# Kernel optimization log

Measured on AMD Instinct MI355X. Metric: run time of the kernel, lower is better.

The kernel has to match this reference:

```python
import jax, jax.numpy as jnp
import numpy as np
import math

T, B, E, H = 1024, 4, 512, 8
HD = E // H

def setup_inputs() -> dict:
    key = jax.random.key(0)
    ks = jax.random.split(key, 6)
    return {
        "query": jax.random.normal(ks[0], (T, B, E), dtype=jnp.float32),
        "dist": jax.random.normal(ks[1], (B, T, T, H), dtype=jnp.float32) * 0.1,
        "in_proj_weight": jax.random.normal(ks[2], (3 * E, E), dtype=jnp.float32) * 0.02,
        "in_proj_bias": jax.random.normal(ks[3], (3 * E,), dtype=jnp.float32) * 0.02,
        "out_proj_weight": jax.random.normal(ks[4], (E, E), dtype=jnp.float32) * 0.02,
        "out_proj_bias": jax.random.normal(ks[5], (E,), dtype=jnp.float32) * 0.02,
    }

def reference(query, dist, in_proj_weight, in_proj_bias, out_proj_weight, out_proj_bias):
    t, b, e = query.shape
    # packed in-projection (self-attention: q=k=v=query)
    qkv = query @ in_proj_weight.T + in_proj_bias          # [T,B,3E]
    q, k, v = jnp.split(qkv, 3, axis=-1)                   # each [T,B,E]
    def heads(x):
        return x.reshape(t, b * H, HD).transpose(1, 0, 2)  # [B*H,T,HD]
    q, k, v = heads(q), heads(k), heads(v)
    q = q / math.sqrt(HD)
    attn = jnp.einsum('bte,bse->bts', q, k)                # [B*H,T,T]
    # distance/structure bias: [B,T,T,H] -> [B,H,T,T] -> [B*H,T,T]
    bias = jnp.transpose(dist, (0, 3, 1, 2)).reshape(b * H, t, t)
    attn = jax.nn.softmax(attn + bias, axis=-1)
    out = jnp.einsum('bts,bse->bte', attn, v)              # [B*H,T,HD]
    out = out.transpose(1, 0, 2).reshape(t, b, e)          # [T,B,E]
    out = out @ out_proj_weight.T + out_proj_bias
    return out
```

## Files before the change

### kernel.cpp

```cpp
#include <hip/hip_runtime.h>
#include <math.h>

typedef __bf16 bf16;
typedef bf16 bf16x8 __attribute__((ext_vector_type(8)));
typedef bf16 bf16x4 __attribute__((ext_vector_type(4)));
typedef float f32x4 __attribute__((ext_vector_type(4)));

#define T_DIM 1024
#define B_DIM 4
#define E_DIM 512
#define H_DIM 8
#define HD_DIM 64
#define BH_DIM 32
#define SPLIT 4
#define S_PER (T_DIM / SPLIT)

__device__ __forceinline__ f32x4 mfma16(bf16x8 a, bf16x8 b, f32x4 c) {
    return __builtin_amdgcn_mfma_f32_16x16x32_bf16(a, b, c, 0, 0, 0);
}

__device__ __forceinline__ bf16x4 cvt4(f32x4 v) {
    bf16x4 o;
    o[0] = (bf16)v[0]; o[1] = (bf16)v[1]; o[2] = (bf16)v[2]; o[3] = (bf16)v[3];
    return o;
}

#define CVT_Q_V   524288
#define CVT_W1_V  196608
__global__ __launch_bounds__(256)
void cvt_all(const float* __restrict__ q, const float* __restrict__ w1,
             const float* __restrict__ w2, bf16* __restrict__ qo,
             bf16* __restrict__ w1o, bf16* __restrict__ w2o) {
    long v = (long)blockIdx.x * 256 + threadIdx.x;
    const float* src; bf16* dst;
    if (v < CVT_Q_V)                { src = q;  dst = qo; }
    else if (v < CVT_Q_V + CVT_W1_V){ v -= CVT_Q_V;  src = w1; dst = w1o; }
    else                            { v -= CVT_Q_V + CVT_W1_V; src = w2; dst = w2o; }
    f32x4 f = *(const f32x4*)(src + v * 4);
    *(bf16x4*)(dst + v * 4) = cvt4(f);
}

__global__ __launch_bounds__(256)
void bias_transpose(const float* __restrict__ dist, bf16* __restrict__ bias_t) {
    __shared__ __align__(16) bf16 tile[8 * 1032];
    const int bt = blockIdx.x;
    const int b = bt >> 10, t = bt & 1023;
    const int tid = threadIdx.x;
    const float* src = dist + ((long)bt << 13) + tid * 32;
    const int s0 = tid * 4;
    float v[32];
#pragma unroll
    for (int j = 0; j < 8; j++) {
        f32x4 f = *(const f32x4*)(src + j * 4);
        v[j * 4 + 0] = f[0]; v[j * 4 + 1] = f[1];
        v[j * 4 + 2] = f[2]; v[j * 4 + 3] = f[3];
    }
#pragma unroll
    for (int h = 0; h < 8; h++)
#pragma unroll
        for (int si = 0; si < 4; si++)
            tile[h * 1032 + s0 + si] = (bf16)v[si * 8 + h];
    __syncthreads();
#pragma unroll
    for (int rep = 0; rep < 4; rep++) {
        int slot = rep * 256 + tid;
        int h = slot >> 7;
        int sc = (slot & 127) * 8;
        bf16x8 o = *(const bf16x8*)&tile[h * 1032 + sc];
        *(bf16x8*)&bias_t[((long)(b * 8 + h) * T_DIM + t) * T_DIM + sc] = o;
    }
}

template<int TM, int TN, int MODE>
__global__ __launch_bounds__(256)
void gemm_t(const bf16* __restrict__ A, const bf16* __restrict__ Bt,
            const float* __restrict__ bias, int K, int N,
            float* __restrict__ out, bf16* __restrict__ qb,
            bf16* __restrict__ kb, bf16* __restrict__ vb) {
    constexpr int FM = TM / 32, FN = TN / 32;
    constexpr int PA = TM / 64, PB = TN / 64;
    __shared__ __align__(16) bf16 As[TM * 72];
    __shared__ __align__(16) bf16 Bs[TN * 72];
    const int tid  = threadIdx.x;
    const int lane = tid & 63;
    const int wave = tid >> 6;
    const int quad = lane >> 4;
    const int l15  = lane & 15;
    const int wm = wave & 1, wn = wave >> 1;
    const int m0 = blockIdx.x * TM, n0 = blockIdx.y * TN;

    f32x4 acc[FM][FN] = {};

    const int sr = tid >> 2;
    const int sc = (tid & 3) * 16;

    bf16x8 ra[PA][2], rb[PB][2];
#pragma unroll
    for (int p = 0; p < PA; p++) {
        const bf16* src = &A[(long)(m0 + p * 64 + sr) * K + sc];
        ra[p][0] = *(const bf16x8*)(src);
        ra[p][1] = *(const bf16x8*)(src + 8);
    }
#pragma unroll
    for (int p = 0; p < PB; p++) {
        const bf16* src = &Bt[(long)(n0 + p * 64 + sr) * K + sc];
        rb[p][0] = *(const bf16x8*)(src);
        rb[p][1] = *(const bf16x8*)(src + 8);
    }

    for (int k0 = 0; k0 < K; k0 += 64) {
        __syncthreads();
#pragma unroll
        for (int p = 0; p < PA; p++) {
            *(bf16x8*)&As[(p * 64 + sr) * 72 + sc]     = ra[p][0];
            *(bf16x8*)&As[(p * 64 + sr) * 72 + sc + 8] = ra[p][1];
        }
#pragma unroll
        for (int p = 0; p < PB; p++) {
            *(bf16x8*)&Bs[(p * 64 + sr) * 72 + sc]     = rb[p][0];
            *(bf16x8*)&Bs[(p * 64 + sr) * 72 + sc + 8] = rb[p][1];
        }
        __syncthreads();

        if (k0 + 64 < K) {
            const int kn = k0 + 64;
#pragma unroll
            for (int p = 0; p < PA; p++) {
                const bf16* src = &A[(long)(m0 + p * 64 + sr) * K + kn + sc];
                ra[p][0] = *(const bf16x8*)(src);
                ra[p][1] = *(const bf16x8*)(src + 8);
            }
#pragma unroll
            for (int p = 0; p < PB; p++) {
                const bf16* src = &Bt[(long)(n0 + p * 64 + sr) * K + kn + sc];
                rb[p][0] = *(const bf16x8*)(src);
                rb[p][1] = *(const bf16x8*)(src + 8);
            }
        }

#pragma unroll
        for (int kk = 0; kk < 64; kk += 32) {
            bf16x8 af[FM], bfr[FN];
#pragma unroll
            for (int mb = 0; mb < FM; mb++)
                af[mb] = *(const bf16x8*)&As[(wm * (TM / 2) + mb * 16 + l15) * 72 + kk + quad * 8];
#pragma unroll
            for (int nb = 0; nb < FN; nb++)
                bfr[nb] = *(const bf16x8*)&Bs[(wn * (TN / 2) + nb * 16 + l15) * 72 + kk + quad * 8];
#pragma unroll
            for (int mb = 0; mb < FM; mb++)
#pragma unroll
                for (int nb = 0; nb < FN; nb++)
                    acc[mb][nb] = mfma16(af[mb], bfr[nb], acc[mb][nb]);
        }
    }

#pragma unroll
    for (int mb = 0; mb < FM; mb++) {
#pragma unroll
        for (int nb = 0; nb < FN; nb++) {
            int n = n0 + wn * (TN / 2) + nb * 16 + l15;
            float bv = bias[n];
#pragma unroll
            for (int r = 0; r < 4; r++) {
                int m = m0 + wm * (TM / 2) + mb * 16 + quad * 4 + r;
                float v = acc[mb][nb][r] + bv;
                if (MODE == 0) {
                    out[(long)m * N + n] = v;
                } else {
                    int t = m >> 2, b = m & 3;
                    int sec = n >> 9, j = n & 511;
                    int h = j >> 6, hd = j & 63;
                    int bh = b * 8 + h;
                    if (sec == 0)
                        qb[((long)bh * T_DIM + t) * HD_DIM + hd] = (bf16)(v * 0.125f);
                    else if (sec == 1)
                        kb[((long)bh * T_DIM + t) * HD_DIM + hd] = (bf16)v;
                    else
                        vb[((long)bh * HD_DIM + hd) * T_DIM + t] = (bf16)v;
                }
            }
        }
    }
}

__global__ __launch_bounds__(256)
void attn_kernel(const bf16* __restrict__ qb, const bf16* __restrict__ kb,
                 const bf16* __restrict__ vb, const bf16* __restrict__ bias_t,
                 float* __restrict__ po, float* __restrict__ pl) {
    __shared__ __align__(16) bf16 Ks[64 * 72];
    __shared__ __align__(16) bf16 Vts[64 * 72];
    __shared__ __align__(16) bf16 Ps[4 * 16 * 72];
    const int tid  = threadIdx.x;
    const int lane = tid & 63;
    const int wave = tid >> 6;
    const int quad = lane >> 4;
    const int l15  = lane & 15;
    const int bid  = blockIdx.x;
    const int bh   = (bid >> 4) & 31;
    const int qt   = bid & 15;
    const int split = bid >> 9;
    const int s0   = split * S_PER;
    const int b    = bh >> 3;
    const int qrow = qt * 64 + wave * 16 + l15;

    bf16x8 qa0 = *(const bf16x8*)&qb[((long)bh * T_DIM + qrow) * HD_DIM + quad * 8];
    bf16x8 qa1 = *(const bf16x8*)&qb[((long)bh * T_DIM + qrow) * HD_DIM + 32 + quad * 8];

    f32x4 oacc[4] = {};
    float lsum[4] = {0.f, 0.f, 0.f, 0.f};

    const int r0 = tid >> 3;
    const int c0 = (tid & 7) * 8;

    const bf16* dp = bias_t + ((long)bh * T_DIM + qt * 64 + wave * 16 + quad * 4) * T_DIM;

    bf16x8 pk0, pk1, pv0, pv1;
    float pbias[16];
    pk0 = *(const bf16x8*)&kb[((long)bh * T_DIM + s0 + r0) * HD_DIM + c0];
    pk1 = *(const bf16x8*)&kb[((long)bh * T_DIM + s0 + r0 + 32) * HD_DIM + c0];
    pv0 = *(const bf16x8*)&vb[((long)bh * HD_DIM + r0) * T_DIM + s0 + c0];
    pv1 = *(const bf16x8*)&vb[((long)bh * HD_DIM + r0 + 32) * T_DIM + s0 + c0];
#pragma unroll
    for (int r = 0; r < 4; r++)
#pragma unroll
        for (int nb = 0; nb < 4; nb++)
            pbias[r * 4 + nb] = (float)dp[(long)r * T_DIM + s0 + nb * 16 + l15];

    for (int st = s0; st < s0 + S_PER; st += 64) {
        __syncthreads();
        *(bf16x8*)&Ks[r0 * 72 + c0]         = pk0;
        *(bf16x8*)&Ks[(r0 + 32) * 72 + c0]  = pk1;
        *(bf16x8*)&Vts[r0 * 72 + c0]        = pv0;
        *(bf16x8*)&Vts[(r0 + 32) * 72 + c0] = pv1;
        __syncthreads();

        if (st + 64 < s0 + S_PER) {
            const int sn = st + 64;
            pk0 = *(const bf16x8*)&kb[((long)bh * T_DIM + sn + r0) * HD_DIM + c0];
            pk1 = *(const bf16x8*)&kb[((long)bh * T_DIM + sn + r0 + 32) * HD_DIM + c0];
            pv0 = *(const bf16x8*)&vb[((long)bh * HD_DIM + r0) * T_DIM + sn + c0];
            pv1 = *(const bf16x8*)&vb[((long)bh * HD_DIM + r0 + 32) * T_DIM + sn + c0];
        }

        f32x4 sacc[4] = {};
        __builtin_amdgcn_s_setprio(1);
#pragma unroll
        for (int kk = 0; kk < 64; kk += 32) {
            bf16x8 a = (kk == 0) ? qa0 : qa1;
#pragma unroll
            for (int nb = 0; nb < 4; nb++) {
                bf16x8 bfr = *(const bf16x8*)&Ks[(nb * 16 + l15) * 72 + kk + quad * 8];
                sacc[nb] = mfma16(a, bfr, sacc[nb]);
            }
        }
        __builtin_amdgcn_s_setprio(0);

        bf16* pw = &Ps[wave * 16 * 72];
#pragma unroll
        for (int r = 0; r < 4; r++) {
            float rs = 0.f;
#pragma unroll
            for (int nb = 0; nb < 4; nb++) {
                float p = __expf(sacc[nb][r] + pbias[r * 4 + nb]);
                rs += p;
                pw[(quad * 4 + r) * 72 + nb * 16 + l15] = (bf16)p;
            }
            lsum[r] += rs;
        }

        if (st + 64 < s0 + S_PER) {
            const int sn = st + 64;
#pragma unroll
            for (int r = 0; r < 4; r++)
#pragma unroll
                for (int nb = 0; nb < 4; nb++)
                    pbias[r * 4 + nb] = (float)dp[(long)r * T_DIM + sn + nb * 16 + l15];
        }

        __builtin_amdgcn_s_setprio(1);
#pragma unroll
        for (int kk = 0; kk < 64; kk += 32) {
            bf16x8 ap = *(const bf16x8*)&pw[l15 * 72 + kk + quad * 8];
#pragma unroll
            for (int nb = 0; nb < 4; nb++) {
                bf16x8 bv2 = *(const bf16x8*)&Vts[(nb * 16 + l15) * 72 + kk + quad * 8];
                oacc[nb] = mfma16(ap, bv2, oacc[nb]);
            }
        }
        __builtin_amdgcn_s_setprio(0);
    }

#pragma unroll
    for (int r = 0; r < 4; r++) {
#pragma unroll
        for (int msk = 1; msk < 16; msk <<= 1)
            lsum[r] += __shfl_xor(lsum[r], msk);
    }

    float* pob = po + (long)split * (BH_DIM * T_DIM * HD_DIM);
#pragma unroll
    for (int nb = 0; nb < 4; nb++) {
#pragma unroll
        for (int r = 0; r < 4; r++) {
            int t  = qt * 64 + wave * 16 + quad * 4 + r;
            int hd = nb * 16 + l15;
            pob[((long)bh * T_DIM + t) * HD_DIM + hd] = oacc[nb][r];
        }
    }
    if (l15 == 0) {
#pragma unroll
        for (int r = 0; r < 4; r++) {
            int t = qt * 64 + wave * 16 + quad * 4 + r;
            pl[(long)split * (BH_DIM * T_DIM) + bh * T_DIM + t] = lsum[r];
        }
    }
}

__global__ __launch_bounds__(256)
void combine(const float* __restrict__ po, const float* __restrict__ pl,
             bf16* __restrict__ ctxb) {
    const int gid = blockIdx.x * 256 + threadIdx.x;
    const int hd4 = gid & 15;
    const int t   = (gid >> 4) & 1023;
    const int bh  = gid >> 14;
    const long base = ((long)bh * T_DIM + t) * HD_DIM + hd4 * 4;
    f32x4 o = {};
    float l = 0.f;
#pragma unroll
    for (int s = 0; s < SPLIT; s++) {
        o += *(const f32x4*)&po[(long)s * (BH_DIM * T_DIM * HD_DIM) + base];
        l += pl[(long)s * (BH_DIM * T_DIM) + bh * T_DIM + t];
    }
    float inv = 1.f / l;
    f32x4 r = o * inv;
    const int b = bh >> 3, hh = bh & 7;
    *(bf16x4*)&ctxb[((long)t * B_DIM + b) * E_DIM + hh * HD_DIM + hd4 * 4] = cvt4(r);
}

extern "C" void kernel_launch(void* const* d_in, const int* in_sizes, int n_in,
                              void* d_out, int out_size, void* d_ws, size_t ws_size,
                              hipStream_t stream) {
    const float* query = (const float*)d_in[0];
    const float* dist  = (const float*)d_in[1];
    const float* win   = (const float*)d_in[2];
    const float* bin   = (const float*)d_in[3];
    const float* wout  = (const float*)d_in[4];
    const float* bout  = (const float*)d_in[5];
    float* out = (float*)d_out;

    bf16* bias_t = (bf16*)d_ws;
    bf16* qb   = bias_t + ((long)BH_DIM * T_DIM * T_DIM);
    bf16* kb   = qb + (1 << 21);
    bf16* vb   = kb + (1 << 21);
    bf16* qbf  = vb + (1 << 21);
    bf16* w1bf = qbf + (1 << 21);
    bf16* w2bf = w1bf + 786432;
    bf16* ctxb = w2bf + 262144;
    float* po  = (float*)(ctxb + (1 << 21));
    float* pl  = po + (long)SPLIT * BH_DIM * T_DIM * HD_DIM;

    cvt_all<<<dim3(3072), 256, 0, stream>>>(query, win, wout, qbf, w1bf, w2bf);
    bias_transpose<<<dim3(B_DIM * T_DIM), 256, 0, stream>>>(dist, bias_t);
    gemm_t<128, 128, 1><<<dim3(32, 12), 256, 0, stream>>>(
        qbf, w1bf, bin, 512, 1536, nullptr, qb, kb, vb);
    attn_kernel<<<dim3(512 * SPLIT), 256, 0, stream>>>(qb, kb, vb, bias_t, po, pl);
    combine<<<dim3(2048), 256, 0, stream>>>(po, pl, ctxb);
    gemm_t<128, 64, 0><<<dim3(32, 8), 256, 0, stream>>>(
        ctxb, w2bf, bout, 512, 512, out, nullptr, nullptr, nullptr);
}
```

Measured before the change: 287.1 us.

## Fuse dist bias transpose into attention kernel and retile projection GEMMs

```diff
diff --git a/kernel.cpp b/kernel.cpp
--- a/kernel.cpp
+++ b/kernel.cpp
@@ -38,37 +38,6 @@
     else                            { v -= CVT_Q_V + CVT_W1_V; src = w2; dst = w2o; }
     f32x4 f = *(const f32x4*)(src + v * 4);
     *(bf16x4*)(dst + v * 4) = cvt4(f);
-}
-
-__global__ __launch_bounds__(256)
-void bias_transpose(const float* __restrict__ dist, bf16* __restrict__ bias_t) {
-    __shared__ __align__(16) bf16 tile[8 * 1032];
-    const int bt = blockIdx.x;
-    const int b = bt >> 10, t = bt & 1023;
-    const int tid = threadIdx.x;
-    const float* src = dist + ((long)bt << 13) + tid * 32;
-    const int s0 = tid * 4;
-    float v[32];
-#pragma unroll
-    for (int j = 0; j < 8; j++) {
-        f32x4 f = *(const f32x4*)(src + j * 4);
-        v[j * 4 + 0] = f[0]; v[j * 4 + 1] = f[1];
-        v[j * 4 + 2] = f[2]; v[j * 4 + 3] = f[3];
-    }
-#pragma unroll
-    for (int h = 0; h < 8; h++)
-#pragma unroll
-        for (int si = 0; si < 4; si++)
-            tile[h * 1032 + s0 + si] = (bf16)v[si * 8 + h];
-    __syncthreads();
-#pragma unroll
-    for (int rep = 0; rep < 4; rep++) {
-        int slot = rep * 256 + tid;
-        int h = slot >> 7;
-        int sc = (slot & 127) * 8;
-        bf16x8 o = *(const bf16x8*)&tile[h * 1032 + sc];
-        *(bf16x8*)&bias_t[((long)(b * 8 + h) * T_DIM + t) * T_DIM + sc] = o;
-    }
 }
 
 template<int TM, int TN, int MODE>
@@ -186,10 +155,9 @@
 
 __global__ __launch_bounds__(256)
 void attn_kernel(const bf16* __restrict__ qb, const bf16* __restrict__ kb,
-                 const bf16* __restrict__ vb, const bf16* __restrict__ bias_t,
+                 const bf16* __restrict__ vb, const float* __restrict__ dist,
                  float* __restrict__ po, float* __restrict__ pl) {
-    __shared__ __align__(16) bf16 Ks[64 * 72];
-    __shared__ __align__(16) bf16 Vts[64 * 72];
+    __shared__ __align__(16) bf16 Bs[8 * 1152];
     __shared__ __align__(16) bf16 Ps[4 * 16 * 72];
     const int tid  = threadIdx.x;
     const int lane = tid & 63;
@@ -197,122 +165,125 @@
     const int quad = lane >> 4;
     const int l15  = lane & 15;
     const int bid  = blockIdx.x;
-    const int bh   = (bid >> 4) & 31;
-    const int qt   = bid & 15;
-    const int split = bid >> 9;
+    const int b    = bid & 3;
+    const int qt   = (bid >> 2) & 63;
+    const int split = bid >> 8;
     const int s0   = split * S_PER;
-    const int b    = bh >> 3;
-    const int qrow = qt * 64 + wave * 16 + l15;
-
-    bf16x8 qa0 = *(const bf16x8*)&qb[((long)bh * T_DIM + qrow) * HD_DIM + quad * 8];
-    bf16x8 qa1 = *(const bf16x8*)&qb[((long)bh * T_DIM + qrow) * HD_DIM + 32 + quad * 8];
-
-    f32x4 oacc[4] = {};
-    float lsum[4] = {0.f, 0.f, 0.f, 0.f};
-
-    const int r0 = tid >> 3;
-    const int c0 = (tid & 7) * 8;
-
-    const bf16* dp = bias_t + ((long)bh * T_DIM + qt * 64 + wave * 16 + quad * 4) * T_DIM;
-
-    bf16x8 pk0, pk1, pv0, pv1;
-    float pbias[16];
-    pk0 = *(const bf16x8*)&kb[((long)bh * T_DIM + s0 + r0) * HD_DIM + c0];
-    pk1 = *(const bf16x8*)&kb[((long)bh * T_DIM + s0 + r0 + 32) * HD_DIM + c0];
-    pv0 = *(const bf16x8*)&vb[((long)bh * HD_DIM + r0) * T_DIM + s0 + c0];
-    pv1 = *(const bf16x8*)&vb[((long)bh * HD_DIM + r0 + 32) * T_DIM + s0 + c0];
-#pragma unroll
-    for (int r = 0; r < 4; r++)
-#pragma unroll
-        for (int nb = 0; nb < 4; nb++)
-            pbias[r * 4 + nb] = (float)dp[(long)r * T_DIM + s0 + nb * 16 + l15];
+    const int t0   = qt * 16;
+
+    bf16x8 qa[2][2];
+#pragma unroll
+    for (int hi = 0; hi < 2; hi++) {
+        const int bh = b * 8 + wave * 2 + hi;
+        const bf16* qp = &qb[((long)bh * T_DIM + t0 + l15) * HD_DIM];
+        qa[hi][0] = *(const bf16x8*)(qp + quad * 8);
+        qa[hi][1] = *(const bf16x8*)(qp + 32 + quad * 8);
+    }
+
+    f32x4 oacc[2][4] = {};
+    float lsum[2][4] = {{0.f,0.f,0.f,0.f},{0.f,0.f,0.f,0.f}};
+
+    const int t_loc = tid >> 4;
+    const int s_loc = (tid & 15) * 4;
+    const float* dsrc = dist + ((long)(b * 1024 + t0 + t_loc) * 1024 + s0) * 8 + s_loc * 8;
+
+    f32x4 dv[8];
+#pragma unroll
+    for (int j = 0; j < 8; j++) dv[j] = *(const f32x4*)(dsrc + j * 4);
 
     for (int st = s0; st < s0 + S_PER; st += 64) {
         __syncthreads();
-        *(bf16x8*)&Ks[r0 * 72 + c0]         = pk0;
-        *(bf16x8*)&Ks[(r0 + 32) * 72 + c0]  = pk1;
-        *(bf16x8*)&Vts[r0 * 72 + c0]        = pv0;
-        *(bf16x8*)&Vts[(r0 + 32) * 72 + c0] = pv1;
+        {
+            const float* vv = (const float*)dv;
+#pragma unroll
+            for (int h = 0; h < 8; h++) {
+                bf16x4 w;
+                w[0] = (bf16)vv[0 * 8 + h];
+                w[1] = (bf16)vv[1 * 8 + h];
+                w[2] = (bf16)vv[2 * 8 + h];
+                w[3] = (bf16)vv[3 * 8 + h];
+                *(bf16x4*)&Bs[h * 1152 + t_loc * 72 + s_loc] = w;
+            }
+        }
         __syncthreads();
 
         if (st + 64 < s0 + S_PER) {
-            const int sn = st + 64;
-            pk0 = *(const bf16x8*)&kb[((long)bh * T_DIM + sn + r0) * HD_DIM + c0];
-            pk1 = *(const bf16x8*)&kb[((long)bh * T_DIM + sn + r0 + 32) * HD_DIM + c0];
-            pv0 = *(const bf16x8*)&vb[((long)bh * HD_DIM + r0) * T_DIM + sn + c0];
-            pv1 = *(const bf16x8*)&vb[((long)bh * HD_DIM + r0 + 32) * T_DIM + sn + c0];
-        }
-
-        f32x4 sacc[4] = {};
-        __builtin_amdgcn_s_setprio(1);
-#pragma unroll
-        for (int kk = 0; kk < 64; kk += 32) {
-            bf16x8 a = (kk == 0) ? qa0 : qa1;
-#pragma unroll
-            for (int nb = 0; nb < 4; nb++) {
-                bf16x8 bfr = *(const bf16x8*)&Ks[(nb * 16 + l15) * 72 + kk + quad * 8];
-                sacc[nb] = mfma16(a, bfr, sacc[nb]);
-            }
-        }
-        __builtin_amdgcn_s_setprio(0);
+            const float* dn = dsrc + (long)(st + 64 - s0) * 8;
+#pragma unroll
+            for (int j = 0; j < 8; j++) dv[j] = *(const f32x4*)(dn + j * 4);
+        }
 
         bf16* pw = &Ps[wave * 16 * 72];
 #pragma unroll
+        for (int hi = 0; hi < 2; hi++) {
+            const int h  = wave * 2 + hi;
+            const int bh = b * 8 + h;
+
+            f32x4 sacc[4] = {};
+            __builtin_amdgcn_s_setprio(1);
+#pragma unroll
+            for (int kk = 0; kk < 64; kk += 32) {
+#pragma unroll
+                for (int nb = 0; nb < 4; nb++) {
+                    bf16x8 kf = *(const bf16x8*)&kb[((long)bh * T_DIM + st + nb * 16 + l15) * HD_DIM + kk + quad * 8];
+                    sacc[nb] = mfma16(qa[hi][kk >> 5], kf, sacc[nb]);
+                }
+            }
+            __builtin_amdgcn_s_setprio(0);
+
+#pragma unroll
+            for (int r = 0; r < 4; r++) {
+                float rs = 0.f;
+#pragma unroll
+                for (int nb = 0; nb < 4; nb++) {
+                    float d = (float)Bs[h * 1152 + (quad * 4 + r) * 72 + nb * 16 + l15];
+                    float p = __expf(sacc[nb][r] + d);
+                    rs += p;
+                    pw[(quad * 4 + r) * 72 + nb * 16 + l15] = (bf16)p;
+                }
+                lsum[hi][r] += rs;
+            }
+
+            __builtin_amdgcn_s_setprio(1);
+#pragma unroll
+            for (int kk = 0; kk < 64; kk += 32) {
+                bf16x8 ap = *(const bf16x8*)&pw[l15 * 72 + kk + quad * 8];
+#pragma unroll
+                for (int nb = 0; nb < 4; nb++) {
+                    bf16x8 vf = *(const bf16x8*)&vb[((long)bh * HD_DIM + nb * 16 + l15) * T_DIM + st + kk + quad * 8];
+                    oacc[hi][nb] = mfma16(ap, vf, oacc[hi][nb]);
+                }
+            }
+            __builtin_amdgcn_s_setprio(0);
+        }
+    }
+
+#pragma unroll
+    for (int hi = 0; hi < 2; hi++)
+#pragma unroll
         for (int r = 0; r < 4; r++) {
-            float rs = 0.f;
-#pragma unroll
-            for (int nb = 0; nb < 4; nb++) {
-                float p = __expf(sacc[nb][r] + pbias[r * 4 + nb]);
-                rs += p;
-                pw[(quad * 4 + r) * 72 + nb * 16 + l15] = (bf16)p;
-            }
-            lsum[r] += rs;
-        }
-
-        if (st + 64 < s0 + S_PER) {
-            const int sn = st + 64;
+#pragma unroll
+            for (int msk = 1; msk < 16; msk <<= 1)
+                lsum[hi][r] += __shfl_xor(lsum[hi][r], msk);
+        }
+
+    float* pob = po + (long)split * (BH_DIM * T_DIM * HD_DIM);
+#pragma unroll
+    for (int hi = 0; hi < 2; hi++) {
+        const int bh = b * 8 + wave * 2 + hi;
+#pragma unroll
+        for (int nb = 0; nb < 4; nb++)
 #pragma unroll
             for (int r = 0; r < 4; r++)
-#pragma unroll
-                for (int nb = 0; nb < 4; nb++)
-                    pbias[r * 4 + nb] = (float)dp[(long)r * T_DIM + sn + nb * 16 + l15];
-        }
-
-        __builtin_amdgcn_s_setprio(1);
-#pragma unroll
-        for (int kk = 0; kk < 64; kk += 32) {
-            bf16x8 ap = *(const bf16x8*)&pw[l15 * 72 + kk + quad * 8];
-#pragma unroll
-            for (int nb = 0; nb < 4; nb++) {
-                bf16x8 bv2 = *(const bf16x8*)&Vts[(nb * 16 + l15) * 72 + kk + quad * 8];
-                oacc[nb] = mfma16(ap, bv2, oacc[nb]);
-            }
-        }
-        __builtin_amdgcn_s_setprio(0);
-    }
-
-#pragma unroll
-    for (int r = 0; r < 4; r++) {
-#pragma unroll
-        for (int msk = 1; msk < 16; msk <<= 1)
-            lsum[r] += __shfl_xor(lsum[r], msk);
-    }
-
-    float* pob = po + (long)split * (BH_DIM * T_DIM * HD_DIM);
-#pragma unroll
-    for (int nb = 0; nb < 4; nb++) {
-#pragma unroll
-        for (int r = 0; r < 4; r++) {
-            int t  = qt * 64 + wave * 16 + quad * 4 + r;
-            int hd = nb * 16 + l15;
-            pob[((long)bh * T_DIM + t) * HD_DIM + hd] = oacc[nb][r];
-        }
+                pob[((long)bh * T_DIM + t0 + quad * 4 + r) * HD_DIM + nb * 16 + l15] = oacc[hi][nb][r];
     }
     if (l15 == 0) {
 #pragma unroll
-        for (int r = 0; r < 4; r++) {
-            int t = qt * 64 + wave * 16 + quad * 4 + r;
-            pl[(long)split * (BH_DIM * T_DIM) + bh * T_DIM + t] = lsum[r];
+        for (int hi = 0; hi < 2; hi++) {
+            const int bh = b * 8 + wave * 2 + hi;
+#pragma unroll
+            for (int r = 0; r < 4; r++)
+                pl[(long)split * (BH_DIM * T_DIM) + bh * T_DIM + t0 + quad * 4 + r] = lsum[hi][r];
         }
     }
 }
@@ -349,8 +320,7 @@
     const float* bout  = (const float*)d_in[5];
     float* out = (float*)d_out;
 
-    bf16* bias_t = (bf16*)d_ws;
-    bf16* qb   = bias_t + ((long)BH_DIM * T_DIM * T_DIM);
+    bf16* qb   = (bf16*)d_ws;
     bf16* kb   = qb + (1 << 21);
     bf16* vb   = kb + (1 << 21);
     bf16* qbf  = vb + (1 << 21);
@@ -361,11 +331,10 @@
     float* pl  = po + (long)SPLIT * BH_DIM * T_DIM * HD_DIM;
 
     cvt_all<<<dim3(3072), 256, 0, stream>>>(query, win, wout, qbf, w1bf, w2bf);
-    bias_transpose<<<dim3(B_DIM * T_DIM), 256, 0, stream>>>(dist, bias_t);
-    gemm_t<128, 128, 1><<<dim3(32, 12), 256, 0, stream>>>(
+    gemm_t<64, 128, 1><<<dim3(64, 12), 256, 0, stream>>>(
         qbf, w1bf, bin, 512, 1536, nullptr, qb, kb, vb);
-    attn_kernel<<<dim3(512 * SPLIT), 256, 0, stream>>>(qb, kb, vb, bias_t, po, pl);
+    attn_kernel<<<dim3(4 * 64 * SPLIT), 256, 0, stream>>>(qb, kb, vb, dist, po, pl);
     combine<<<dim3(2048), 256, 0, stream>>>(po, pl, ctxb);
-    gemm_t<128, 64, 0><<<dim3(32, 8), 256, 0, stream>>>(
+    gemm_t<64, 64, 0><<<dim3(64, 8), 256, 0, stream>>>(
         ctxb, w2bf, bout, 512, 512, out, nullptr, nullptr, nullptr);
 }
```

Result: slower. 293.0 us (+2.1%).
